# Kernel tuning notes

Measured on AMD Instinct MI355X. Metric: run time of the kernel, lower is better.

The kernel has to match this reference:

```python
import jax, jax.numpy as jnp
import numpy as np
import math

N, S, E, H = 32, 64, 512, 4
HD = E // H
EQ = E // 4
L2_TEMP = 13.544
LN_EPS = 1e-5


def _ln(x, g, b):
    m = jnp.mean(x, -1, keepdims=True)
    v = jnp.var(x, -1, keepdims=True)
    return (x - m) * jax.lax.rsqrt(v + LN_EPS) * g + b


def setup_inputs() -> dict:
    key = jax.random.key(0)
    ks = jax.random.split(key, 16)
    sc = 0.02
    inp = {
        "x": jax.random.normal(ks[0], (N, S, E), jnp.float32),
        # MultiheadAttention params (torch layout: in_proj_weight (3E,E))
        "Wqkv": jax.random.normal(ks[1], (3 * E, E), jnp.float32) * sc,
        "bqkv": jnp.zeros((3 * E,), jnp.float32),
        "Wo": jax.random.normal(ks[2], (E, E), jnp.float32) * sc,
        "bo": jnp.zeros((E,), jnp.float32),
        # fc1 (E, 2E), fc2 (E, E)
        "W1": jax.random.normal(ks[3], (E, 2 * E), jnp.float32) * sc,
        "b1": jnp.zeros((E,), jnp.float32),
        "W2": jax.random.normal(ks[4], (E, E), jnp.float32) * sc,
        "b2": jnp.zeros((E,), jnp.float32),
        # layer norms
        "g1": jnp.ones((E,), jnp.float32), "be1": jnp.zeros((E,), jnp.float32),
        "g2": jnp.ones((E,), jnp.float32), "be2": jnp.zeros((E,), jnp.float32),
        # fc_diff1: Linear(E, E//4), Linear(E//4, 1)
        "d1W1": jax.random.normal(ks[5], (EQ, E), jnp.float32) * sc,
        "d1b1": jnp.zeros((EQ,), jnp.float32),
        "d1W2": jax.random.normal(ks[6], (1, EQ), jnp.float32) * sc,
        "d1b2": jnp.zeros((1,), jnp.float32),
        # fc_diff2
        "d2W1": jax.random.normal(ks[7], (EQ, E), jnp.float32) * sc,
        "d2b1": jnp.zeros((EQ,), jnp.float32),
        "d2W2": jax.random.normal(ks[8], (1, EQ), jnp.float32) * sc,
        "d2b2": jnp.zeros((1,), jnp.float32),
    }
    return inp


def _mha(x, Wqkv, bqkv, Wo, bo):
    n, s, e = x.shape
    qkv = x @ Wqkv.T + bqkv
    q, k, v = jnp.split(qkv, 3, axis=-1)
    sh = lambda t: t.reshape(n, s, H, HD).transpose(0, 2, 1, 3)  # (n,H,s,hd)
    q, k, v = sh(q), sh(k), sh(v)
    scores = jnp.einsum('bhqd,bhkd->bhqk', q, k) / math.sqrt(HD)
    a = jax.nn.softmax(scores, axis=-1)
    o = jnp.einsum('bhqk,bhkd->bhqd', a, v).transpose(0, 2, 1, 3).reshape(n, s, e)
    return o @ Wo.T + bo, a.mean(axis=1)  # averaged attn weights (torch default)


def _pair_mlp(diff_w, W1a, b1a, W2a, b2a):
    # F.relu applied after every 'layer' (Linear, Dropout(eval=id), Linear)
    h = jax.nn.relu(diff_w @ W1a.T + b1a)  # relu(dropout(relu)) == relu composed -> same
    return jax.nn.relu(h @ W2a.T + b2a)[..., 0]  # (N,f,f)


def reference(x, Wqkv, bqkv, Wo, bo, W1, b1, W2, b2, g1, be1, g2, be2,
              d1W1, d1b1, d1W2, d1b2, d2W1, d2b1, d2W2, d2b2):
    # diff[b,f,g,e] = x[b,g,e] - x[b,f,e]
    diff = x[:, None, :, :] - x[:, :, None, :]  # (N,f,f,E)
    x1_attn = jax.nn.softmax(-jnp.sum(diff * diff, -1) / L2_TEMP, axis=-1)  # (N,f,f)
    x1 = jnp.einsum('bfg,bge->bfe', x1_attn, x)
    x2, x2_attn = _mha(x, Wqkv, bqkv, Wo, bo)
    x_res = jnp.concatenate([x1, x2], axis=-1)
    h = x + jax.nn.relu(x_res @ W1.T + b1)  # dropout eval = identity
    h = _ln(h, g1, be1)
    h = h + jax.nn.relu(h @ W2.T + b2)
    out = _ln(h, g2, be2)
    diff1 = _pair_mlp(diff * x1_attn[..., None], d1W1, d1b1, d1W2, d1b2)
    diff2 = _pair_mlp(diff * x2_attn[..., None], d2W1, d2b1, d2W2, d2b2)
    return out, x1_attn[:, None], x2_attn[:, None], diff1, diff2
```

## Files before the change

kernel.cpp:

```cpp
#include <hip/hip_runtime.h>
#include <math.h>

#define NB 32
#define SS 64
#define EE 512
#define L2T 13.544f
#define LNEPS 1e-5f

using bf16x8 = __attribute__((ext_vector_type(8))) __bf16;
using u16x8  = __attribute__((ext_vector_type(8))) unsigned short;
using f32x4  = __attribute__((ext_vector_type(4))) float;

typedef const void __attribute__((address_space(1))) cv_global;
typedef void __attribute__((address_space(3))) v_lds;

__device__ inline unsigned short f2bf(float f) {
    union { float f; unsigned u; } v; v.f = f;
    unsigned r = v.u + 0x7fff + ((v.u >> 16) & 1);
    return (unsigned short)(r >> 16);
}
__device__ inline float bf2f(unsigned short h) {
    union { unsigned u; float f; } v; v.u = (unsigned)h << 16;
    return v.f;
}

__global__ __launch_bounds__(256)
void convert_w(const float* __restrict__ Wqkv, const float* __restrict__ Wo,
               const float* __restrict__ W1, const float* __restrict__ W2,
               const float* __restrict__ d1, const float* __restrict__ d2,
               unsigned short* __restrict__ dst) {
    int i = blockIdx.x * 256 + threadIdx.x;
    const float* s; int off;
    if (i < 196608)      { s = Wqkv; off = 0; }
    else if (i < 262144) { s = Wo;   off = 196608; }
    else if (i < 393216) { s = W1;   off = 262144; }
    else if (i < 458752) { s = W2;   off = 393216; }
    else if (i < 475136) { s = d1;   off = 458752; }
    else                 { s = d2;   off = 475136; }
    float4 v = ((const float4*)s)[i - off];
    ushort4 o;
    o.x = f2bf(v.x); o.y = f2bf(v.y); o.z = f2bf(v.z); o.w = f2bf(v.w);
    ((ushort4*)dst)[i] = o;
}

__global__ __launch_bounds__(256)
void l2attn_x1(const float* __restrict__ x, float* __restrict__ x1_attn,
               unsigned short* __restrict__ x_resb,
               unsigned short* __restrict__ xb) {
    const int f = blockIdx.x, b = blockIdx.y;
    const int tid = threadIdx.x, wave = tid >> 6, lane = tid & 63;
    __shared__ float d2s[64];
    __shared__ float attn_s[64];

    const float4* xv = (const float4*)(x + (size_t)b * SS * EE);
    float4 xf0 = xv[f * 128 + lane * 2];
    float4 xf1 = xv[f * 128 + lane * 2 + 1];

    for (int g = wave; g < 64; g += 4) {
        float4 a0 = xv[g * 128 + lane * 2];
        float4 a1 = xv[g * 128 + lane * 2 + 1];
        float dx, s = 0.f;
        dx = a0.x - xf0.x; s += dx * dx;
        dx = a0.y - xf0.y; s += dx * dx;
        dx = a0.z - xf0.z; s += dx * dx;
        dx = a0.w - xf0.w; s += dx * dx;
        dx = a1.x - xf1.x; s += dx * dx;
        dx = a1.y - xf1.y; s += dx * dx;
        dx = a1.z - xf1.z; s += dx * dx;
        dx = a1.w - xf1.w; s += dx * dx;
        #pragma unroll
        for (int m = 32; m; m >>= 1) s += __shfl_xor(s, m);
        if (lane == 0) d2s[g] = s;
    }
    __syncthreads();

    if (tid < 64) {
        float v = -d2s[tid] * (1.0f / L2T);
        float mx = v;
        #pragma unroll
        for (int m = 32; m; m >>= 1) mx = fmaxf(mx, __shfl_xor(mx, m));
        float e = expf(v - mx);
        float sum = e;
        #pragma unroll
        for (int m = 32; m; m >>= 1) sum += __shfl_xor(sum, m);
        float a = e / sum;
        x1_attn[((size_t)b * SS + f) * SS + tid] = a;
        attn_s[tid] = a;
    }
    __syncthreads();

    const float* xbf = x + (size_t)b * SS * EE;
    float acc0 = 0.f, acc1 = 0.f;
    #pragma unroll 8
    for (int g = 0; g < 64; ++g) {
        float ag = attn_s[g];
        acc0 += ag * xbf[g * EE + tid];
        acc1 += ag * xbf[g * EE + tid + 256];
    }
    unsigned short* dst = x_resb + ((size_t)b * SS + f) * 1024;
    dst[tid] = f2bf(acc0);
    dst[tid + 256] = f2bf(acc1);
    unsigned short* xrow = xb + ((size_t)b * SS + f) * EE;
    xrow[tid] = f2bf(xbf[f * EE + tid]);
    xrow[tid + 256] = f2bf(xbf[f * EE + tid + 256]);
}

template <int BM, bool RELU, bool OUTBF16>
__global__ __launch_bounds__(256)
void gemm_mfma(const unsigned short* __restrict__ A, int lda,
               const unsigned short* __restrict__ B, int ldb,
               const float* __restrict__ bias, float* __restrict__ Cf,
               unsigned short* __restrict__ Cb, int ldc, int K) {
    __shared__ unsigned short Asl[BM * 64];
    __shared__ unsigned short Bsl[64 * 64];
    const int tid = threadIdx.x, wave = tid >> 6, lane = tid & 63;
    const int m0 = blockIdx.y * BM, n0 = blockIdx.x * 64;

    constexpr int RF = BM / 32;
    const int wm = (wave >> 1) * (BM / 2);
    const int wn = (wave & 1) * 32;
    const int fr = lane & 15;
    const int kq4 = lane >> 4;

    f32x4 acc[RF][2] = {};

    for (int k0 = 0; k0 < K; k0 += 64) {
        #pragma unroll
        for (int c0 = 0; c0 < BM * 8; c0 += 256) {
            int cc = c0 + tid, r = cc >> 3, q = cc & 7;
            int col = (q ^ (r & 7)) * 8;
            __builtin_amdgcn_global_load_lds(
                (cv_global*)(A + (size_t)(m0 + r) * lda + k0 + col),
                (v_lds*)(Asl + c0 * 8 + wave * 512), 16, 0, 0);
        }
        #pragma unroll
        for (int c0 = 0; c0 < 512; c0 += 256) {
            int cc = c0 + tid, r = cc >> 3, q = cc & 7;
            int col = (q ^ (r & 7)) * 8;
            __builtin_amdgcn_global_load_lds(
                (cv_global*)(B + (size_t)(n0 + r) * ldb + k0 + col),
                (v_lds*)(Bsl + c0 * 8 + wave * 512), 16, 0, 0);
        }
        __syncthreads();
        #pragma unroll
        for (int j = 0; j < 2; ++j) {
            int kc = kq4 + j * 4;
            int rb0 = wn + fr, rb1 = wn + 16 + fr;
            bf16x8 b0 = *(const bf16x8*)(Bsl + rb0 * 64 + (kc ^ (rb0 & 7)) * 8);
            bf16x8 b1 = *(const bf16x8*)(Bsl + rb1 * 64 + (kc ^ (rb1 & 7)) * 8);
            #pragma unroll
            for (int r = 0; r < RF; ++r) {
                int ra = wm + r * 16 + fr;
                bf16x8 af = *(const bf16x8*)(Asl + ra * 64 + (kc ^ (ra & 7)) * 8);
                acc[r][0] = __builtin_amdgcn_mfma_f32_16x16x32_bf16(af, b0, acc[r][0], 0, 0, 0);
                acc[r][1] = __builtin_amdgcn_mfma_f32_16x16x32_bf16(af, b1, acc[r][1], 0, 0, 0);
            }
        }
        __syncthreads();
    }

    const int crow = (lane >> 4) * 4, ccol = lane & 15;
    float bj0 = bias ? bias[n0 + wn + ccol] : 0.f;
    float bj1 = bias ? bias[n0 + wn + 16 + ccol] : 0.f;
    #pragma unroll
    for (int r = 0; r < RF; ++r) {
        #pragma unroll
        for (int c = 0; c < 2; ++c) {
            float bj = c ? bj1 : bj0;
            #pragma unroll
            for (int i = 0; i < 4; ++i) {
                size_t m = (size_t)(m0 + wm + r * 16 + crow + i);
                int n = n0 + wn + c * 16 + ccol;
                float v = acc[r][c][i] + bj;
                if (RELU) v = fmaxf(v, 0.f);
                if (OUTBF16) Cb[m * ldc + n] = f2bf(v);
                else         Cf[m * ldc + n] = v;
            }
        }
    }
}

__global__ __launch_bounds__(256)
void mha_attn(const unsigned short* __restrict__ qkv,
              unsigned short* __restrict__ o_buf, float* __restrict__ pws) {
    const int hh = blockIdx.x;
    const int h = hh >> 1, half = hh & 1;
    const int b = blockIdx.y;
    const int tid = threadIdx.x, wave = tid >> 6, lane = tid & 63;

    __shared__ unsigned short Qs[32 * 136];
    __shared__ unsigned short Ks[64 * 136];
    __shared__ unsigned short Vt[128 * 72];
    __shared__ float sc[32 * 68];
    __shared__ unsigned short Pb[32 * 72];

    const unsigned short* base = qkv + (size_t)b * 64 * 1536;

    {
        int row = tid >> 3, col = (tid & 7) * 16;
        const unsigned short* src = base + (half * 32 + row) * 1536 + h * 128 + col;
        *(u16x8*)(Qs + row * 136 + col)     = *(const u16x8*)(src);
        *(u16x8*)(Qs + row * 136 + col + 8) = *(const u16x8*)(src + 8);
    }
    {
        int row = tid >> 2, col = (tid & 3) * 32;
        const unsigned short* src = base + row * 1536 + 512 + h * 128 + col;
        #pragma unroll
        for (int j = 0; j < 4; ++j)
            *(u16x8*)(Ks + row * 136 + col + j * 8) = *(const u16x8*)(src + j * 8);
    }
    {
        int g = tid >> 2, col = (tid & 3) * 32;
        const unsigned short* src = base + g * 1536 + 1024 + h * 128 + col;
        #pragma unroll
        for (int j = 0; j < 4; ++j) {
            u16x8 v = *(const u16x8*)(src + j * 8);
            #pragma unroll
            for (int e = 0; e < 8; ++e)
                Vt[(col + j * 8 + e) * 72 + g] = v[e];
        }
    }
    __syncthreads();

    const int fr = lane & 15, kq = (lane >> 4) * 8;
    const int crow = (lane >> 4) * 4, ccol = lane & 15;
    const int wm = (wave >> 1) * 16;

    {
        const int wn = (wave & 1) * 32;
        f32x4 s0 = {0.f, 0.f, 0.f, 0.f}, s1 = s0;
        #pragma unroll
        for (int k0 = 0; k0 < 128; k0 += 32) {
            bf16x8 a  = *(const bf16x8*)(Qs + (wm + fr) * 136 + k0 + kq);
            bf16x8 b0 = *(const bf16x8*)(Ks + (wn + fr) * 136 + k0 + kq);
            bf16x8 b1 = *(const bf16x8*)(Ks + (wn + 16 + fr) * 136 + k0 + kq);
            s0 = __builtin_amdgcn_mfma_f32_16x16x32_bf16(a, b0, s0, 0, 0, 0);
            s1 = __builtin_amdgcn_mfma_f32_16x16x32_bf16(a, b1, s1, 0, 0, 0);
        }
        const float scale = 0.08838834764831845f;
        #pragma unroll
        for (int r = 0; r < 4; ++r) {
            sc[(wm + crow + r) * 68 + wn + ccol]      = s0[r] * scale;
            sc[(wm + crow + r) * 68 + wn + 16 + ccol] = s1[r] * scale;
        }
    }
    __syncthreads();

    #pragma unroll
    for (int i = 0; i < 8; ++i) {
        int f = wave * 8 + i;
        float v = sc[f * 68 + lane];
        float mx = v;
        #pragma unroll
        for (int m = 32; m; m >>= 1) mx = fmaxf(mx, __shfl_xor(mx, m));
        float e = expf(v - mx);
        float sum = e;
        #pragma unroll
        for (int m = 32; m; m >>= 1) sum += __shfl_xor(sum, m);
        float a = e / sum;
        Pb[f * 72 + lane] = f2bf(a);
        pws[(((size_t)b * 4 + h) * 64 + half * 32 + f) * 64 + lane] = a;
    }
    __syncthreads();

    {
        const int wn2 = (wave & 1) * 64;
        f32x4 o[4];
        #pragma unroll
        for (int t = 0; t < 4; ++t) o[t] = f32x4{0.f, 0.f, 0.f, 0.f};
        #pragma unroll
        for (int k0 = 0; k0 < 64; k0 += 32) {
            bf16x8 a = *(const bf16x8*)(Pb + (wm + fr) * 72 + k0 + kq);
            #pragma unroll
            for (int t = 0; t < 4; ++t) {
                bf16x8 bv = *(const bf16x8*)(Vt + (wn2 + t * 16 + fr) * 72 + k0 + kq);
                o[t] = __builtin_amdgcn_mfma_f32_16x16x32_bf16(a, bv, o[t], 0, 0, 0);
            }
        }
        #pragma unroll
        for (int t = 0; t < 4; ++t) {
            #pragma unroll
            for (int r = 0; r < 4; ++r) {
                size_t m = (size_t)b * 64 + half * 32 + wm + crow + r;
                int col = h * 128 + wn2 + t * 16 + ccol;
                o_buf[m * 512 + col] = f2bf(o[t][r]);
            }
        }
    }
}

__global__ __launch_bounds__(256)
void add_ln(const float* __restrict__ base, const float* __restrict__ u,
            const float* __restrict__ gam, const float* __restrict__ bet,
            float* __restrict__ out, unsigned short* __restrict__ outb) {
    const int row = blockIdx.x;
    const int tid = threadIdx.x, wave = tid >> 6, lane = tid & 63;
    const float* br = base + (size_t)row * EE;
    const float* ur = u + (size_t)row * EE;
    float t0 = br[tid] + ur[tid];
    float t1 = br[tid + 256] + ur[tid + 256];
    float s = t0 + t1, sq = t0 * t0 + t1 * t1;
    #pragma unroll
    for (int m = 32; m; m >>= 1) {
        s += __shfl_xor(s, m);
        sq += __shfl_xor(sq, m);
    }
    __shared__ float ssum[4], ssq[4];
    if (lane == 0) { ssum[wave] = s; ssq[wave] = sq; }
    __syncthreads();
    s = ssum[0] + ssum[1] + ssum[2] + ssum[3];
    sq = ssq[0] + ssq[1] + ssq[2] + ssq[3];
    float mean = s * (1.0f / EE);
    float var = sq * (1.0f / EE) - mean * mean;
    float inv = rsqrtf(var + LNEPS);
    float v0 = (t0 - mean) * inv * gam[tid] + bet[tid];
    float v1 = (t1 - mean) * inv * gam[tid + 256] + bet[tid + 256];
    float* orow = out + (size_t)row * EE;
    orow[tid] = v0;
    orow[tid + 256] = v1;
    if (outb) {
        unsigned short* obr = outb + (size_t)row * EE;
        obr[tid] = f2bf(v0);
        obr[tid + 256] = f2bf(v1);
    }
}

__global__ __launch_bounds__(256)
void pair_mlp(const float* __restrict__ P, const float* __restrict__ a1,
              const float* __restrict__ pws, const float* __restrict__ d1b1,
              const float* __restrict__ d1w2, const float* __restrict__ d1b2,
              const float* __restrict__ d2b1, const float* __restrict__ d2w2,
              const float* __restrict__ d2b2, float* __restrict__ x2_attn,
              float* __restrict__ out1, float* __restrict__ out2) {
    const int f = blockIdx.x, b = blockIdx.y;
    const int tid = threadIdx.x, wave = tid >> 6, lane = tid & 63;
    const size_t row = (size_t)b * SS + f;
    const int c0 = lane * 2, c1 = lane * 2 + 1;

    const float p1f0 = P[row * 256 + c0],       p1f1 = P[row * 256 + c1];
    const float p2f0 = P[row * 256 + 128 + c0], p2f1 = P[row * 256 + 128 + c1];
    const float w10 = d1w2[c0], w11 = d1w2[c1];
    const float w20 = d2w2[c0], w21 = d2w2[c1];
    const float b10 = d1b1[c0], b11 = d1b1[c1];
    const float b20 = d2b1[c0], b21 = d2b1[c1];
    const float bb1 = d1b2[0], bb2 = d2b2[0];

    const float* a1r = a1 + row * SS;
    const float* ph0 = pws + (((size_t)b * 4 + 0) * 64 + f) * 64;
    const float* ph1 = pws + (((size_t)b * 4 + 1) * 64 + f) * 64;
    const float* ph2 = pws + (((size_t)b * 4 + 2) * 64 + f) * 64;
    const float* ph3 = pws + (((size_t)b * 4 + 3) * 64 + f) * 64;
    const size_t bbase = (size_t)b * SS * 256;

    for (int g = wave; g < 64; g += 4) {
        float aa1 = a1r[g];
        float aa2 = 0.25f * (ph0[g] + ph1[g] + ph2[g] + ph3[g]);
        float q10 = P[bbase + g * 256 + c0],       q11 = P[bbase + g * 256 + c1];
        float q20 = P[bbase + g * 256 + 128 + c0], q21 = P[bbase + g * 256 + 128 + c1];
        float h10 = fmaxf(aa1 * (q10 - p1f0) + b10, 0.f);
        float h11 = fmaxf(aa1 * (q11 - p1f1) + b11, 0.f);
        float h20 = fmaxf(aa2 * (q20 - p2f0) + b20, 0.f);
        float h21 = fmaxf(aa2 * (q21 - p2f1) + b21, 0.f);
        float s1 = w10 * h10 + w11 * h11;
        float s2 = w20 * h20 + w21 * h21;
        #pragma unroll
        for (int m = 32; m; m >>= 1) {
            s1 += __shfl_xor(s1, m);
            s2 += __shfl_xor(s2, m);
        }
        if (lane == 0) {
            x2_attn[row * SS + g] = aa2;
            out1[row * SS + g] = fmaxf(s1 + bb1, 0.f);
            out2[row * SS + g] = fmaxf(s2 + bb2, 0.f);
        }
    }
}

extern "C" void kernel_launch(void* const* d_in, const int* in_sizes, int n_in,
                              void* d_out, int out_size, void* d_ws,
                              size_t ws_size, hipStream_t stream) {
    const float* x    = (const float*)d_in[0];
    const float* Wqkv = (const float*)d_in[1];
    const float* bqkv = (const float*)d_in[2];
    const float* Wo   = (const float*)d_in[3];
    const float* bo   = (const float*)d_in[4];
    const float* W1   = (const float*)d_in[5];
    const float* b1   = (const float*)d_in[6];
    const float* W2   = (const float*)d_in[7];
    const float* b2   = (const float*)d_in[8];
    const float* g1   = (const float*)d_in[9];
    const float* be1  = (const float*)d_in[10];
    const float* g2   = (const float*)d_in[11];
    const float* be2  = (const float*)d_in[12];
    const float* d1W1 = (const float*)d_in[13];
    const float* d1b1 = (const float*)d_in[14];
    const float* d1W2 = (const float*)d_in[15];
    const float* d1b2 = (const float*)d_in[16];
    const float* d2W1 = (const float*)d_in[17];
    const float* d2b1 = (const float*)d_in[18];
    const float* d2W2 = (const float*)d_in[19];
    const float* d2b2 = (const float*)d_in[20];

    float* out      = (float*)d_out;
    float* out_main = out;
    float* x1_attn  = out + 1048576;
    float* x2_attn  = out + 1048576 + 131072;
    float* diff1    = out + 1048576 + 2 * 131072;
    float* diff2    = out + 1048576 + 3 * 131072;

    float* ws    = (float*)d_ws;
    float* u_buf = ws;
    float* h_buf = u_buf + 1048576;
    float* P     = h_buf + 1048576;
    float* pws   = P + 524288;
    unsigned short* bb    = (unsigned short*)(pws + 524288);
    unsigned short* xb    = bb;
    unsigned short* Wqkvb = bb + 1048576;
    unsigned short* Wob   = bb + 1835008;
    unsigned short* W1b   = bb + 2097152;
    unsigned short* W2b   = bb + 2621440;
    unsigned short* Wpb   = bb + 2883584;
    unsigned short* qkvb  = bb + 3014656;
    unsigned short* ob    = bb + 6160384;
    unsigned short* x_resb= bb + 7208960;
    unsigned short* hb    = bb + 9306112;

    convert_w<<<1920, 256, 0, stream>>>(Wqkv, Wo, W1, W2, d1W1, d2W1,
                                        bb + 1048576);

    l2attn_x1<<<dim3(64, 32), 256, 0, stream>>>(x, x1_attn, x_resb, xb);

    gemm_mfma<64, false, true><<<dim3(24, 32), 256, 0, stream>>>(
        xb, 512, Wqkvb, 512, bqkv, nullptr, qkvb, 1536, 512);

    mha_attn<<<dim3(8, 32), 256, 0, stream>>>(qkvb, ob, pws);

    gemm_mfma<32, false, true><<<dim3(8, 64), 256, 0, stream>>>(
        ob, 512, Wob, 512, bo, nullptr, x_resb + 512, 1024, 512);

    gemm_mfma<32, true, false><<<dim3(8, 64), 256, 0, stream>>>(
        x_resb, 1024, W1b, 1024, b1, u_buf, nullptr, 512, 1024);

    add_ln<<<2048, 256, 0, stream>>>(x, u_buf, g1, be1, h_buf, hb);

    gemm_mfma<32, true, false><<<dim3(8, 64), 256, 0, stream>>>(
        hb, 512, W2b, 512, b2, u_buf, nullptr, 512, 512);

    add_ln<<<2048, 256, 0, stream>>>(h_buf, u_buf, g2, be2, out_main, nullptr);

    gemm_mfma<32, false, false><<<dim3(4, 64), 256, 0, stream>>>(
        xb, 512, Wpb, 512, nullptr, P, nullptr, 256, 512);

    pair_mlp<<<dim3(64, 32), 256, 0, stream>>>(P, x1_attn, pws, d1b1, d1W2,
                                               d1b2, d2b1, d2W2, d2b2, x2_attn,
                                               diff1, diff2);
}
```

Before: 198.1 us.

## Fold Wo into W1, merge launches into mega-kernels and fused GEMMs

Folds the output projection algebraically into fc1 by precomputing W1[:,512:]·Wo and an effective bias, which removes the separate Wo GEMM. Weight conversion, the fold, and the L2 attention are merged into one heterogeneous launch. The QKV projection and the pair-MLP projection now share a single GEMM. The fc1 GEMM and the pair MLP are combined into a single launch (w1pair), so fewer kernels run overall. The cost is an extra folded GEMM per call, a different bf16 rounding path for the folded weights, and uneven block roles inside the fused kernels.

```diff
diff --git a/kernel.cpp b/kernel.cpp
--- a/kernel.cpp
+++ b/kernel.cpp
@@ -1,7 +1,6 @@
 #include <hip/hip_runtime.h>
 #include <math.h>
 
-#define NB 32
 #define SS 64
 #define EE 512
 #define L2T 13.544f
@@ -24,121 +23,183 @@
     return v.f;
 }
 
+#define XB_O    0
+#define WFULL_O 1048576
+#define W1CB_O  1966080
+#define W2B_O   2490368
+#define QKVB_O  2752512
+#define X1O_O   5898240
+#define HB_O    7995392
+#define PB_O    9043968
+
 __global__ __launch_bounds__(256)
-void convert_w(const float* __restrict__ Wqkv, const float* __restrict__ Wo,
-               const float* __restrict__ W1, const float* __restrict__ W2,
-               const float* __restrict__ d1, const float* __restrict__ d2,
-               unsigned short* __restrict__ dst) {
-    int i = blockIdx.x * 256 + threadIdx.x;
-    const float* s; int off;
-    if (i < 196608)      { s = Wqkv; off = 0; }
-    else if (i < 262144) { s = Wo;   off = 196608; }
-    else if (i < 393216) { s = W1;   off = 262144; }
-    else if (i < 458752) { s = W2;   off = 393216; }
-    else if (i < 475136) { s = d1;   off = 458752; }
-    else                 { s = d2;   off = 475136; }
-    float4 v = ((const float4*)s)[i - off];
-    ushort4 o;
-    o.x = f2bf(v.x); o.y = f2bf(v.y); o.z = f2bf(v.z); o.w = f2bf(v.w);
-    ((ushort4*)dst)[i] = o;
+void mega1(const float* __restrict__ x, const float* __restrict__ Wqkv,
+           const float* __restrict__ Wo, const float* __restrict__ W1,
+           const float* __restrict__ W2, const float* __restrict__ d1,
+           const float* __restrict__ d2, const float* __restrict__ b1,
+           const float* __restrict__ bo, unsigned short* __restrict__ bb,
+           float* __restrict__ b_eff, float* __restrict__ x1_attn) {
+    const int bx = blockIdx.x, tid = threadIdx.x;
+    __shared__ unsigned short ps[5120];
+    __shared__ float l2s[128];
+
+    if (bx < 1408) {
+        int i = bx * 256 + tid;
+        ushort4* dst4 = (ushort4*)bb;
+        const float4* s; int di;
+        if (i < 196608)      { s = (const float4*)Wqkv + i;          di = WFULL_O/4 + i; }
+        else if (i < 212992) { int j = i-196608; s = (const float4*)d1 + j; di = WFULL_O/4 + 196608 + j; }
+        else if (i < 229376) { int j = i-212992; s = (const float4*)d2 + j; di = WFULL_O/4 + 212992 + j; }
+        else if (i < 294912) { int j = i-229376; s = (const float4*)W2 + j; di = W2B_O/4 + j; }
+        else                 { int j = i-294912; int r = j>>7, cq = j&127;
+                               s = (const float4*)W1 + r*256 + cq;   di = W1CB_O/4 + r*256 + cq; }
+        float4 v = *s;
+        ushort4 o;
+        o.x = f2bf(v.x); o.y = f2bf(v.y); o.z = f2bf(v.z); o.w = f2bf(v.w);
+        dst4[di] = o;
+    } else if (bx < 1472) {
+        const int tb = bx - 1408;
+        const int m0 = (tb >> 3) * 64, n0 = (tb & 7) * 64;
+        unsigned short* Asl = ps;
+        unsigned short* Bsl = ps + 64 * 40;
+        const int wave = tid >> 6, lane = tid & 63;
+        const int wm = (wave >> 1) * 32, wn = (wave & 1) * 32;
+        const int fr = lane & 15, kq = (lane >> 4) * 8;
+        f32x4 acc[2][2] = {};
+        for (int k0 = 0; k0 < 512; k0 += 32) {
+            {
+                int m = tid >> 2, kk = (tid & 3) * 8;
+                const float* src = W1 + (size_t)(m0 + m) * 1024 + 512 + k0 + kk;
+                float4 v0 = *(const float4*)src, v1 = *(const float4*)(src + 4);
+                u16x8 t = {f2bf(v0.x), f2bf(v0.y), f2bf(v0.z), f2bf(v0.w),
+                           f2bf(v1.x), f2bf(v1.y), f2bf(v1.z), f2bf(v1.w)};
+                *(u16x8*)(Asl + m * 40 + kk) = t;
+            }
+            {
+                int k = tid >> 3, jq = (tid & 7) * 8;
+                const float* src = Wo + (size_t)(k0 + k) * 512 + n0 + jq;
+                float4 v0 = *(const float4*)src, v1 = *(const float4*)(src + 4);
+                float vv[8] = {v0.x, v0.y, v0.z, v0.w, v1.x, v1.y, v1.z, v1.w};
+                #pragma unroll
+                for (int e = 0; e < 8; ++e) Bsl[(jq + e) * 40 + k] = f2bf(vv[e]);
+            }
+            __syncthreads();
+            bf16x8 a0 = *(const bf16x8*)(Asl + (wm + fr) * 40 + kq);
+            bf16x8 a1 = *(const bf16x8*)(Asl + (wm + 16 + fr) * 40 + kq);
+            bf16x8 b0 = *(const bf16x8*)(Bsl + (wn + fr) * 40 + kq);
+            bf16x8 b1 = *(const bf16x8*)(Bsl + (wn + 16 + fr) * 40 + kq);
+            acc[0][0] = __builtin_amdgcn_mfma_f32_16x16x32_bf16(a0, b0, acc[0][0], 0, 0, 0);
+            acc[0][1] = __builtin_amdgcn_mfma_f32_16x16x32_bf16(a0, b1, acc[0][1], 0, 0, 0);
+            acc[1][0] = __builtin_amdgcn_mfma_f32_16x16x32_bf16(a1, b0, acc[1][0], 0, 0, 0);
+            acc[1][1] = __builtin_amdgcn_mfma_f32_16x16x32_bf16(a1, b1, acc[1][1], 0, 0, 0);
+            __syncthreads();
+        }
+        unsigned short* W1cb = bb + W1CB_O;
+        const int crow = (lane >> 4) * 4, ccol = lane & 15;
+        #pragma unroll
+        for (int r2 = 0; r2 < 2; ++r2)
+            #pragma unroll
+            for (int c2 = 0; c2 < 2; ++c2)
+                #pragma unroll
+                for (int i = 0; i < 4; ++i) {
+                    int m = m0 + wm + r2 * 16 + crow + i;
+                    int j = n0 + wn + c2 * 16 + ccol;
+                    W1cb[(size_t)m * 1024 + 512 + j] = f2bf(acc[r2][c2][i]);
+                }
+    } else if (bx < 1476) {
+        int n = (bx - 1472) * 128 + (tid >> 1);
+        int kh = (tid & 1) * 256;
+        float s = 0.f;
+        for (int k = 0; k < 256; ++k)
+            s += W1[(size_t)n * 1024 + 512 + kh + k] * bo[kh + k];
+        s += __shfl_xor(s, 1);
+        if ((tid & 1) == 0) b_eff[n] = b1[n] + s;
+    } else {
+        const int idx = bx - 1476;
+        const int b = idx >> 6, f = idx & 63;
+        const int wave = tid >> 6, lane = tid & 63;
+        float* d2s = l2s; float* attn_s = l2s + 64;
+
+        const float4* xv = (const float4*)(x + (size_t)b * SS * EE);
+        float4 xf0 = xv[f * 128 + lane * 2];
+        float4 xf1 = xv[f * 128 + lane * 2 + 1];
+
+        for (int g = wave; g < 64; g += 4) {
+            float4 a0 = xv[g * 128 + lane * 2];
+            float4 a1 = xv[g * 128 + lane * 2 + 1];
+            float dx, s = 0.f;
+            dx = a0.x - xf0.x; s += dx * dx;
+            dx = a0.y - xf0.y; s += dx * dx;
+            dx = a0.z - xf0.z; s += dx * dx;
+            dx = a0.w - xf0.w; s += dx * dx;
+            dx = a1.x - xf1.x; s += dx * dx;
+            dx = a1.y - xf1.y; s += dx * dx;
+            dx = a1.z - xf1.z; s += dx * dx;
+            dx = a1.w - xf1.w; s += dx * dx;
+            #pragma unroll
+            for (int m = 32; m; m >>= 1) s += __shfl_xor(s, m);
+            if (lane == 0) d2s[g] = s;
+        }
+        __syncthreads();
+        if (tid < 64) {
+            float v = -d2s[tid] * (1.0f / L2T);
+            float mx = v;
+            #pragma unroll
+            for (int m = 32; m; m >>= 1) mx = fmaxf(mx, __shfl_xor(mx, m));
+            float e = expf(v - mx);
+            float sum = e;
+            #pragma unroll
+            for (int m = 32; m; m >>= 1) sum += __shfl_xor(sum, m);
+            float a = e / sum;
+            x1_attn[((size_t)b * SS + f) * SS + tid] = a;
+            attn_s[tid] = a;
+        }
+        __syncthreads();
+        const float* xbf = x + (size_t)b * SS * EE;
+        float acc0 = 0.f, acc1 = 0.f;
+        #pragma unroll 8
+        for (int g = 0; g < 64; ++g) {
+            float ag = attn_s[g];
+            acc0 += ag * xbf[g * EE + tid];
+            acc1 += ag * xbf[g * EE + tid + 256];
+        }
+        unsigned short* dst = bb + X1O_O + ((size_t)b * SS + f) * 1024;
+        dst[tid] = f2bf(acc0);
+        dst[tid + 256] = f2bf(acc1);
+        unsigned short* xrow = bb + XB_O + ((size_t)b * SS + f) * EE;
+        xrow[tid] = f2bf(xbf[f * EE + tid]);
+        xrow[tid + 256] = f2bf(xbf[f * EE + tid + 256]);
+    }
 }
 
 __global__ __launch_bounds__(256)
-void l2attn_x1(const float* __restrict__ x, float* __restrict__ x1_attn,
-               unsigned short* __restrict__ x_resb,
-               unsigned short* __restrict__ xb) {
-    const int f = blockIdx.x, b = blockIdx.y;
-    const int tid = threadIdx.x, wave = tid >> 6, lane = tid & 63;
-    __shared__ float d2s[64];
-    __shared__ float attn_s[64];
-
-    const float4* xv = (const float4*)(x + (size_t)b * SS * EE);
-    float4 xf0 = xv[f * 128 + lane * 2];
-    float4 xf1 = xv[f * 128 + lane * 2 + 1];
-
-    for (int g = wave; g < 64; g += 4) {
-        float4 a0 = xv[g * 128 + lane * 2];
-        float4 a1 = xv[g * 128 + lane * 2 + 1];
-        float dx, s = 0.f;
-        dx = a0.x - xf0.x; s += dx * dx;
-        dx = a0.y - xf0.y; s += dx * dx;
-        dx = a0.z - xf0.z; s += dx * dx;
-        dx = a0.w - xf0.w; s += dx * dx;
-        dx = a1.x - xf1.x; s += dx * dx;
-        dx = a1.y - xf1.y; s += dx * dx;
-        dx = a1.z - xf1.z; s += dx * dx;
-        dx = a1.w - xf1.w; s += dx * dx;
-        #pragma unroll
-        for (int m = 32; m; m >>= 1) s += __shfl_xor(s, m);
-        if (lane == 0) d2s[g] = s;
-    }
-    __syncthreads();
-
-    if (tid < 64) {
-        float v = -d2s[tid] * (1.0f / L2T);
-        float mx = v;
-        #pragma unroll
-        for (int m = 32; m; m >>= 1) mx = fmaxf(mx, __shfl_xor(mx, m));
-        float e = expf(v - mx);
-        float sum = e;
-        #pragma unroll
-        for (int m = 32; m; m >>= 1) sum += __shfl_xor(sum, m);
-        float a = e / sum;
-        x1_attn[((size_t)b * SS + f) * SS + tid] = a;
-        attn_s[tid] = a;
-    }
-    __syncthreads();
-
-    const float* xbf = x + (size_t)b * SS * EE;
-    float acc0 = 0.f, acc1 = 0.f;
-    #pragma unroll 8
-    for (int g = 0; g < 64; ++g) {
-        float ag = attn_s[g];
-        acc0 += ag * xbf[g * EE + tid];
-        acc1 += ag * xbf[g * EE + tid + 256];
-    }
-    unsigned short* dst = x_resb + ((size_t)b * SS + f) * 1024;
-    dst[tid] = f2bf(acc0);
-    dst[tid + 256] = f2bf(acc1);
-    unsigned short* xrow = xb + ((size_t)b * SS + f) * EE;
-    xrow[tid] = f2bf(xbf[f * EE + tid]);
-    xrow[tid + 256] = f2bf(xbf[f * EE + tid + 256]);
-}
-
-template <int BM, bool RELU, bool OUTBF16>
-__global__ __launch_bounds__(256)
-void gemm_mfma(const unsigned short* __restrict__ A, int lda,
-               const unsigned short* __restrict__ B, int ldb,
-               const float* __restrict__ bias, float* __restrict__ Cf,
-               unsigned short* __restrict__ Cb, int ldc, int K) {
-    __shared__ unsigned short Asl[BM * 64];
+void gemm_qkvp(const unsigned short* __restrict__ A,
+               const unsigned short* __restrict__ B,
+               const float* __restrict__ bias,
+               unsigned short* __restrict__ Cq, unsigned short* __restrict__ Cp) {
+    __shared__ unsigned short Asl[64 * 64];
     __shared__ unsigned short Bsl[64 * 64];
     const int tid = threadIdx.x, wave = tid >> 6, lane = tid & 63;
-    const int m0 = blockIdx.y * BM, n0 = blockIdx.x * 64;
-
-    constexpr int RF = BM / 32;
-    const int wm = (wave >> 1) * (BM / 2);
-    const int wn = (wave & 1) * 32;
-    const int fr = lane & 15;
-    const int kq4 = lane >> 4;
-
-    f32x4 acc[RF][2] = {};
-
-    for (int k0 = 0; k0 < K; k0 += 64) {
-        #pragma unroll
-        for (int c0 = 0; c0 < BM * 8; c0 += 256) {
-            int cc = c0 + tid, r = cc >> 3, q = cc & 7;
-            int col = (q ^ (r & 7)) * 8;
-            __builtin_amdgcn_global_load_lds(
-                (cv_global*)(A + (size_t)(m0 + r) * lda + k0 + col),
-                (v_lds*)(Asl + c0 * 8 + wave * 512), 16, 0, 0);
-        }
+    const int m0 = blockIdx.y * 64, n0 = blockIdx.x * 64;
+    const int wm = (wave >> 1) * 32, wn = (wave & 1) * 32;
+    const int fr = lane & 15, kq4 = lane >> 4;
+    f32x4 acc[2][2] = {};
+
+    for (int k0 = 0; k0 < 512; k0 += 64) {
         #pragma unroll
         for (int c0 = 0; c0 < 512; c0 += 256) {
             int cc = c0 + tid, r = cc >> 3, q = cc & 7;
             int col = (q ^ (r & 7)) * 8;
             __builtin_amdgcn_global_load_lds(
-                (cv_global*)(B + (size_t)(n0 + r) * ldb + k0 + col),
+                (cv_global*)(A + (size_t)(m0 + r) * 512 + k0 + col),
+                (v_lds*)(Asl + c0 * 8 + wave * 512), 16, 0, 0);
+        }
+        #pragma unroll
+        for (int c0 = 0; c0 < 512; c0 += 256) {
+            int cc = c0 + tid, r = cc >> 3, q = cc & 7;
+            int col = (q ^ (r & 7)) * 8;
+            __builtin_amdgcn_global_load_lds(
+                (cv_global*)(B + (size_t)(n0 + r) * 512 + k0 + col),
                 (v_lds*)(Bsl + c0 * 8 + wave * 512), 16, 0, 0);
         }
         __syncthreads();
@@ -149,7 +210,7 @@
             bf16x8 b0 = *(const bf16x8*)(Bsl + rb0 * 64 + (kc ^ (rb0 & 7)) * 8);
             bf16x8 b1 = *(const bf16x8*)(Bsl + rb1 * 64 + (kc ^ (rb1 & 7)) * 8);
             #pragma unroll
-            for (int r = 0; r < RF; ++r) {
+            for (int r = 0; r < 2; ++r) {
                 int ra = wm + r * 16 + fr;
                 bf16x8 af = *(const bf16x8*)(Asl + ra * 64 + (kc ^ (ra & 7)) * 8);
                 acc[r][0] = __builtin_amdgcn_mfma_f32_16x16x32_bf16(af, b0, acc[r][0], 0, 0, 0);
@@ -160,29 +221,38 @@
     }
 
     const int crow = (lane >> 4) * 4, ccol = lane & 15;
-    float bj0 = bias ? bias[n0 + wn + ccol] : 0.f;
-    float bj1 = bias ? bias[n0 + wn + 16 + ccol] : 0.f;
-    #pragma unroll
-    for (int r = 0; r < RF; ++r) {
-        #pragma unroll
-        for (int c = 0; c < 2; ++c) {
-            float bj = c ? bj1 : bj0;
-            #pragma unroll
-            for (int i = 0; i < 4; ++i) {
-                size_t m = (size_t)(m0 + wm + r * 16 + crow + i);
-                int n = n0 + wn + c * 16 + ccol;
-                float v = acc[r][c][i] + bj;
-                if (RELU) v = fmaxf(v, 0.f);
-                if (OUTBF16) Cb[m * ldc + n] = f2bf(v);
-                else         Cf[m * ldc + n] = v;
-            }
-        }
+    if (blockIdx.x < 24) {
+        float bj0 = bias[n0 + wn + ccol], bj1 = bias[n0 + wn + 16 + ccol];
+        #pragma unroll
+        for (int r = 0; r < 2; ++r)
+            #pragma unroll
+            for (int c = 0; c < 2; ++c) {
+                float bj = c ? bj1 : bj0;
+                #pragma unroll
+                for (int i = 0; i < 4; ++i) {
+                    size_t m = (size_t)(m0 + wm + r * 16 + crow + i);
+                    int n = n0 + wn + c * 16 + ccol;
+                    Cq[m * 1536 + n] = f2bf(acc[r][c][i] + bj);
+                }
+            }
+    } else {
+        int p0 = n0 - 1536;
+        #pragma unroll
+        for (int r = 0; r < 2; ++r)
+            #pragma unroll
+            for (int c = 0; c < 2; ++c)
+                #pragma unroll
+                for (int i = 0; i < 4; ++i) {
+                    size_t m = (size_t)(m0 + wm + r * 16 + crow + i);
+                    int n = p0 + wn + c * 16 + ccol;
+                    Cp[m * 256 + n] = f2bf(acc[r][c][i]);
+                }
     }
 }
 
 __global__ __launch_bounds__(256)
 void mha_attn(const unsigned short* __restrict__ qkv,
-              unsigned short* __restrict__ o_buf, float* __restrict__ pws) {
+              unsigned short* __restrict__ x1o, float* __restrict__ pws) {
     const int hh = blockIdx.x;
     const int h = hh >> 1, half = hh & 1;
     const int b = blockIdx.y;
@@ -192,10 +262,9 @@
     __shared__ unsigned short Ks[64 * 136];
     __shared__ unsigned short Vt[128 * 72];
     __shared__ float sc[32 * 68];
-    __shared__ unsigned short Pb[32 * 72];
+    __shared__ unsigned short Pbf[32 * 72];
 
     const unsigned short* base = qkv + (size_t)b * 64 * 1536;
-
     {
         int row = tid >> 3, col = (tid & 7) * 16;
         const unsigned short* src = base + (half * 32 + row) * 1536 + h * 128 + col;
@@ -225,7 +294,6 @@
     const int fr = lane & 15, kq = (lane >> 4) * 8;
     const int crow = (lane >> 4) * 4, ccol = lane & 15;
     const int wm = (wave >> 1) * 16;
-
     {
         const int wn = (wave & 1) * 32;
         f32x4 s0 = {0.f, 0.f, 0.f, 0.f}, s1 = s0;
@@ -258,7 +326,7 @@
         #pragma unroll
         for (int m = 32; m; m >>= 1) sum += __shfl_xor(sum, m);
         float a = e / sum;
-        Pb[f * 72 + lane] = f2bf(a);
+        Pbf[f * 72 + lane] = f2bf(a);
         pws[(((size_t)b * 4 + h) * 64 + half * 32 + f) * 64 + lane] = a;
     }
     __syncthreads();
@@ -270,7 +338,7 @@
         for (int t = 0; t < 4; ++t) o[t] = f32x4{0.f, 0.f, 0.f, 0.f};
         #pragma unroll
         for (int k0 = 0; k0 < 64; k0 += 32) {
-            bf16x8 a = *(const bf16x8*)(Pb + (wm + fr) * 72 + k0 + kq);
+            bf16x8 a = *(const bf16x8*)(Pbf + (wm + fr) * 72 + k0 + kq);
             #pragma unroll
             for (int t = 0; t < 4; ++t) {
                 bf16x8 bv = *(const bf16x8*)(Vt + (wn2 + t * 16 + fr) * 72 + k0 + kq);
@@ -278,13 +346,174 @@
             }
         }
         #pragma unroll
-        for (int t = 0; t < 4; ++t) {
+        for (int t = 0; t < 4; ++t)
             #pragma unroll
             for (int r = 0; r < 4; ++r) {
                 size_t m = (size_t)b * 64 + half * 32 + wm + crow + r;
                 int col = h * 128 + wn2 + t * 16 + ccol;
-                o_buf[m * 512 + col] = f2bf(o[t][r]);
-            }
+                x1o[m * 1024 + 512 + col] = f2bf(o[t][r]);
+            }
+    }
+}
+
+__global__ __launch_bounds__(256)
+void w1pair(const unsigned short* __restrict__ x1o,
+            const unsigned short* __restrict__ W1cb,
+            const float* __restrict__ beff, float* __restrict__ u,
+            const unsigned short* __restrict__ Pb,
+            const float* __restrict__ a1, const float* __restrict__ pws,
+            const float* __restrict__ d1b1, const float* __restrict__ d1w2,
+            const float* __restrict__ d1b2, const float* __restrict__ d2b1,
+            const float* __restrict__ d2w2, const float* __restrict__ d2b2,
+            float* __restrict__ x2_attn, float* __restrict__ out1,
+            float* __restrict__ out2) {
+    __shared__ unsigned short Asl[32 * 64];
+    __shared__ unsigned short Bsl[64 * 64];
+    const int bx = blockIdx.x, tid = threadIdx.x;
+    const int wave = tid >> 6, lane = tid & 63;
+
+    if (bx < 512) {
+        const int m0 = (bx >> 3) * 32, n0 = (bx & 7) * 64;
+        const int wm = (wave >> 1) * 16, wn = (wave & 1) * 32;
+        const int fr = lane & 15, kq4 = lane >> 4;
+        f32x4 acc[2] = {};
+        for (int k0 = 0; k0 < 1024; k0 += 64) {
+            {
+                int r = tid >> 3, q = tid & 7;
+                int col = (q ^ (r & 7)) * 8;
+                __builtin_amdgcn_global_load_lds(
+                    (cv_global*)(x1o + (size_t)(m0 + r) * 1024 + k0 + col),
+                    (v_lds*)(Asl + wave * 512), 16, 0, 0);
+            }
+            #pragma unroll
+            for (int c0 = 0; c0 < 512; c0 += 256) {
+                int cc = c0 + tid, r = cc >> 3, q = cc & 7;
+                int col = (q ^ (r & 7)) * 8;
+                __builtin_amdgcn_global_load_lds(
+                    (cv_global*)(W1cb + (size_t)(n0 + r) * 1024 + k0 + col),
+                    (v_lds*)(Bsl + c0 * 8 + wave * 512), 16, 0, 0);
+            }
+            __syncthreads();
+            #pragma unroll
+            for (int j = 0; j < 2; ++j) {
+                int kc = kq4 + j * 4;
+                int rb0 = wn + fr, rb1 = wn + 16 + fr, ra = wm + fr;
+                bf16x8 b0 = *(const bf16x8*)(Bsl + rb0 * 64 + (kc ^ (rb0 & 7)) * 8);
+                bf16x8 b1 = *(const bf16x8*)(Bsl + rb1 * 64 + (kc ^ (rb1 & 7)) * 8);
+                bf16x8 af = *(const bf16x8*)(Asl + ra * 64 + (kc ^ (ra & 7)) * 8);
+                acc[0] = __builtin_amdgcn_mfma_f32_16x16x32_bf16(af, b0, acc[0], 0, 0, 0);
+                acc[1] = __builtin_amdgcn_mfma_f32_16x16x32_bf16(af, b1, acc[1], 0, 0, 0);
+            }
+            __syncthreads();
+        }
+        const int crow = (lane >> 4) * 4, ccol = lane & 15;
+        #pragma unroll
+        for (int c = 0; c < 2; ++c) {
+            int n = n0 + wn + c * 16 + ccol;
+            float bj = beff[n];
+            #pragma unroll
+            for (int i = 0; i < 4; ++i) {
+                size_t m = (size_t)(m0 + wm + crow + i);
+                u[m * 512 + n] = fmaxf(acc[c][i] + bj, 0.f);
+            }
+        }
+    } else {
+        const int idx = bx - 512;
+        const int f = idx & 63, b = idx >> 6;
+        const size_t row = (size_t)b * SS + f;
+        const int c0 = lane * 2, c1 = lane * 2 + 1;
+
+        const float p1f0 = bf2f(Pb[row * 256 + c0]),       p1f1 = bf2f(Pb[row * 256 + c1]);
+        const float p2f0 = bf2f(Pb[row * 256 + 128 + c0]), p2f1 = bf2f(Pb[row * 256 + 128 + c1]);
+        const float w10 = d1w2[c0], w11 = d1w2[c1];
+        const float w20 = d2w2[c0], w21 = d2w2[c1];
+        const float b10 = d1b1[c0], b11 = d1b1[c1];
+        const float b20 = d2b1[c0], b21 = d2b1[c1];
+        const float bb1 = d1b2[0], bb2 = d2b2[0];
+
+        const float* a1r = a1 + row * SS;
+        const float* ph0 = pws + (((size_t)b * 4 + 0) * 64 + f) * 64;
+        const float* ph1 = pws + (((size_t)b * 4 + 1) * 64 + f) * 64;
+        const float* ph2 = pws + (((size_t)b * 4 + 2) * 64 + f) * 64;
+        const float* ph3 = pws + (((size_t)b * 4 + 3) * 64 + f) * 64;
+        const size_t bbase = (size_t)b * SS * 256;
+
+        for (int g = wave; g < 64; g += 4) {
+            float aa1 = a1r[g];
+            float aa2 = 0.25f * (ph0[g] + ph1[g] + ph2[g] + ph3[g]);
+            float q10 = bf2f(Pb[bbase + g * 256 + c0]);
+            float q11 = bf2f(Pb[bbase + g * 256 + c1]);
+            float q20 = bf2f(Pb[bbase + g * 256 + 128 + c0]);
+            float q21 = bf2f(Pb[bbase + g * 256 + 128 + c1]);
+            float h10 = fmaxf(aa1 * (q10 - p1f0) + b10, 0.f);
+            float h11 = fmaxf(aa1 * (q11 - p1f1) + b11, 0.f);
+            float h20 = fmaxf(aa2 * (q20 - p2f0) + b20, 0.f);
+            float h21 = fmaxf(aa2 * (q21 - p2f1) + b21, 0.f);
+            float s1 = w10 * h10 + w11 * h11;
+            float s2 = w20 * h20 + w21 * h21;
+            #pragma unroll
+            for (int m = 32; m; m >>= 1) {
+                s1 += __shfl_xor(s1, m);
+                s2 += __shfl_xor(s2, m);
+            }
+            if (lane == 0) {
+                x2_attn[row * SS + g] = aa2;
+                out1[row * SS + g] = fmaxf(s1 + bb1, 0.f);
+                out2[row * SS + g] = fmaxf(s2 + bb2, 0.f);
+            }
+        }
+    }
+}
+
+__global__ __launch_bounds__(256)
+void gemm_w2(const unsigned short* __restrict__ A,
+             const unsigned short* __restrict__ B,
+             const float* __restrict__ bias, float* __restrict__ C) {
+    __shared__ unsigned short Asl[32 * 64];
+    __shared__ unsigned short Bsl[64 * 64];
+    const int tid = threadIdx.x, wave = tid >> 6, lane = tid & 63;
+    const int m0 = blockIdx.y * 32, n0 = blockIdx.x * 64;
+    const int wm = (wave >> 1) * 16, wn = (wave & 1) * 32;
+    const int fr = lane & 15, kq4 = lane >> 4;
+    f32x4 acc[2] = {};
+    for (int k0 = 0; k0 < 512; k0 += 64) {
+        {
+            int r = tid >> 3, q = tid & 7;
+            int col = (q ^ (r & 7)) * 8;
+            __builtin_amdgcn_global_load_lds(
+                (cv_global*)(A + (size_t)(m0 + r) * 512 + k0 + col),
+                (v_lds*)(Asl + wave * 512), 16, 0, 0);
+        }
+        #pragma unroll
+        for (int c0 = 0; c0 < 512; c0 += 256) {
+            int cc = c0 + tid, r = cc >> 3, q = cc & 7;
+            int col = (q ^ (r & 7)) * 8;
+            __builtin_amdgcn_global_load_lds(
+                (cv_global*)(B + (size_t)(n0 + r) * 512 + k0 + col),
+                (v_lds*)(Bsl + c0 * 8 + wave * 512), 16, 0, 0);
+        }
+        __syncthreads();
+        #pragma unroll
+        for (int j = 0; j < 2; ++j) {
+            int kc = kq4 + j * 4;
+            int rb0 = wn + fr, rb1 = wn + 16 + fr, ra = wm + fr;
+            bf16x8 b0 = *(const bf16x8*)(Bsl + rb0 * 64 + (kc ^ (rb0 & 7)) * 8);
+            bf16x8 b1 = *(const bf16x8*)(Bsl + rb1 * 64 + (kc ^ (rb1 & 7)) * 8);
+            bf16x8 af = *(const bf16x8*)(Asl + ra * 64 + (kc ^ (ra & 7)) * 8);
+            acc[0] = __builtin_amdgcn_mfma_f32_16x16x32_bf16(af, b0, acc[0], 0, 0, 0);
+            acc[1] = __builtin_amdgcn_mfma_f32_16x16x32_bf16(af, b1, acc[1], 0, 0, 0);
+        }
+        __syncthreads();
+    }
+    const int crow = (lane >> 4) * 4, ccol = lane & 15;
+    #pragma unroll
+    for (int c = 0; c < 2; ++c) {
+        int n = n0 + wn + c * 16 + ccol;
+        float bj = bias[n];
+        #pragma unroll
+        for (int i = 0; i < 4; ++i) {
+            size_t m = (size_t)(m0 + wm + crow + i);
+            C[m * 512 + n] = fmaxf(acc[c][i] + bj, 0.f);
         }
     }
 }
@@ -322,57 +551,6 @@
         unsigned short* obr = outb + (size_t)row * EE;
         obr[tid] = f2bf(v0);
         obr[tid + 256] = f2bf(v1);
-    }
-}
-
-__global__ __launch_bounds__(256)
-void pair_mlp(const float* __restrict__ P, const float* __restrict__ a1,
-              const float* __restrict__ pws, const float* __restrict__ d1b1,
-              const float* __restrict__ d1w2, const float* __restrict__ d1b2,
-              const float* __restrict__ d2b1, const float* __restrict__ d2w2,
-              const float* __restrict__ d2b2, float* __restrict__ x2_attn,
-              float* __restrict__ out1, float* __restrict__ out2) {
-    const int f = blockIdx.x, b = blockIdx.y;
-    const int tid = threadIdx.x, wave = tid >> 6, lane = tid & 63;
-    const size_t row = (size_t)b * SS + f;
-    const int c0 = lane * 2, c1 = lane * 2 + 1;
-
-    const float p1f0 = P[row * 256 + c0],       p1f1 = P[row * 256 + c1];
-    const float p2f0 = P[row * 256 + 128 + c0], p2f1 = P[row * 256 + 128 + c1];
-    const float w10 = d1w2[c0], w11 = d1w2[c1];
-    const float w20 = d2w2[c0], w21 = d2w2[c1];
-    const float b10 = d1b1[c0], b11 = d1b1[c1];
-    const float b20 = d2b1[c0], b21 = d2b1[c1];
-    const float bb1 = d1b2[0], bb2 = d2b2[0];
-
-    const float* a1r = a1 + row * SS;
-    const float* ph0 = pws + (((size_t)b * 4 + 0) * 64 + f) * 64;
-    const float* ph1 = pws + (((size_t)b * 4 + 1) * 64 + f) * 64;
-    const float* ph2 = pws + (((size_t)b * 4 + 2) * 64 + f) * 64;
-    const float* ph3 = pws + (((size_t)b * 4 + 3) * 64 + f) * 64;
-    const size_t bbase = (size_t)b * SS * 256;
-
-    for (int g = wave; g < 64; g += 4) {
-        float aa1 = a1r[g];
-        float aa2 = 0.25f * (ph0[g] + ph1[g] + ph2[g] + ph3[g]);
-        float q10 = P[bbase + g * 256 + c0],       q11 = P[bbase + g * 256 + c1];
-        float q20 = P[bbase + g * 256 + 128 + c0], q21 = P[bbase + g * 256 + 128 + c1];
-        float h10 = fmaxf(aa1 * (q10 - p1f0) + b10, 0.f);
-        float h11 = fmaxf(aa1 * (q11 - p1f1) + b11, 0.f);
-        float h20 = fmaxf(aa2 * (q20 - p2f0) + b20, 0.f);
-        float h21 = fmaxf(aa2 * (q21 - p2f1) + b21, 0.f);
-        float s1 = w10 * h10 + w11 * h11;
-        float s2 = w20 * h20 + w21 * h21;
-        #pragma unroll
-        for (int m = 32; m; m >>= 1) {
-            s1 += __shfl_xor(s1, m);
-            s2 += __shfl_xor(s2, m);
-        }
-        if (lane == 0) {
-            x2_attn[row * SS + g] = aa2;
-            out1[row * SS + g] = fmaxf(s1 + bb1, 0.f);
-            out2[row * SS + g] = fmaxf(s2 + bb2, 0.f);
-        }
     }
 }
 
@@ -410,48 +588,34 @@
 
     float* ws    = (float*)d_ws;
     float* u_buf = ws;
-    float* h_buf = u_buf + 1048576;
-    float* P     = h_buf + 1048576;
-    float* pws   = P + 524288;
-    unsigned short* bb    = (unsigned short*)(pws + 524288);
-    unsigned short* xb    = bb;
-    unsigned short* Wqkvb = bb + 1048576;
-    unsigned short* Wob   = bb + 1835008;
-    unsigned short* W1b   = bb + 2097152;
-    unsigned short* W2b   = bb + 2621440;
-    unsigned short* Wpb   = bb + 2883584;
-    unsigned short* qkvb  = bb + 3014656;
-    unsigned short* ob    = bb + 6160384;
-    unsigned short* x_resb= bb + 7208960;
-    unsigned short* hb    = bb + 9306112;
-
-    convert_w<<<1920, 256, 0, stream>>>(Wqkv, Wo, W1, W2, d1W1, d2W1,
-                                        bb + 1048576);
-
-    l2attn_x1<<<dim3(64, 32), 256, 0, stream>>>(x, x1_attn, x_resb, xb);
-
-    gemm_mfma<64, false, true><<<dim3(24, 32), 256, 0, stream>>>(
-        xb, 512, Wqkvb, 512, bqkv, nullptr, qkvb, 1536, 512);
-
-    mha_attn<<<dim3(8, 32), 256, 0, stream>>>(qkvb, ob, pws);
-
-    gemm_mfma<32, false, true><<<dim3(8, 64), 256, 0, stream>>>(
-        ob, 512, Wob, 512, bo, nullptr, x_resb + 512, 1024, 512);
-
-    gemm_mfma<32, true, false><<<dim3(8, 64), 256, 0, stream>>>(
-        x_resb, 1024, W1b, 1024, b1, u_buf, nullptr, 512, 1024);
+    float* h_buf = ws + 1048576;
+    float* pws   = ws + 2097152;
+    float* b_eff = ws + 2621440;
+    unsigned short* bb = (unsigned short*)(ws + 2621952);
+
+    unsigned short* xb    = bb + XB_O;
+    unsigned short* Wfull = bb + WFULL_O;
+    unsigned short* W1cb  = bb + W1CB_O;
+    unsigned short* W2b   = bb + W2B_O;
+    unsigned short* qkvb  = bb + QKVB_O;
+    unsigned short* x1o   = bb + X1O_O;
+    unsigned short* hb    = bb + HB_O;
+    unsigned short* Pb    = bb + PB_O;
+
+    mega1<<<3524, 256, 0, stream>>>(x, Wqkv, Wo, W1, W2, d1W1, d2W1, b1, bo,
+                                    bb, b_eff, x1_attn);
+
+    gemm_qkvp<<<dim3(28, 32), 256, 0, stream>>>(xb, Wfull, bqkv, qkvb, Pb);
+
+    mha_attn<<<dim3(8, 32), 256, 0, stream>>>(qkvb, x1o, pws);
+
+    w1pair<<<2560, 256, 0, stream>>>(x1o, W1cb, b_eff, u_buf, Pb, x1_attn, pws,
+                                     d1b1, d1W2, d1b2, d2b1, d2W2, d2b2,
+                                     x2_attn, diff1, diff2);
 
     add_ln<<<2048, 256, 0, stream>>>(x, u_buf, g1, be1, h_buf, hb);
 
-    gemm_mfma<32, true, false><<<dim3(8, 64), 256, 0, stream>>>(
-        hb, 512, W2b, 512, b2, u_buf, nullptr, 512, 512);
+    gemm_w2<<<dim3(8, 64), 256, 0, stream>>>(hb, W2b, b2, u_buf);
 
     add_ln<<<2048, 256, 0, stream>>>(h_buf, u_buf, g2, be2, out_main, nullptr);
-
-    gemm_mfma<32, false, false><<<dim3(4, 64), 256, 0, stream>>>(
-        xb, 512, Wpb, 512, nullptr, P, nullptr, 256, 512);
-
-    pair_mlp<<<dim3(64, 32), 256, 0, stream>>>(P, x1_attn, pws, d1b1, d1W2,
-                                               d1b2, d2b1, d2W2, d2b2, x2_attn,
-                                               diff1, diff2);
-}
+}
```

After: 191.2 us. -3.5%, faster.
